# Kernel tuning notes

Hardware: AMD Instinct MI355X
Metric: run time of the kernel (lower is better)

## Reference

```python
import jax, jax.numpy as jnp
import numpy as np

QMAX = 127.0  # int8 symmetric range


def fake_quant(t):
    """Per-tensor symmetric int8 quantize->dequantize (HMQ-style numerics)."""
    scale = jnp.maximum(jnp.max(jnp.abs(t)), 1e-8) / QMAX
    q = jnp.clip(jnp.round(t / scale), -QMAX, QMAX)
    return q * scale


def hmq_linear(x, w, b):
    # quantize activations and weights, dequantized GEMM + bias
    xq = fake_quant(x)
    wq = fake_quant(w)
    return jnp.einsum('bsi,oi->bso', xq, wq) + b


def setup_inputs() -> dict:
    key = jax.random.key(0)
    k = jax.random.split(key, 5)
    d, h = 1024, 4096
    return {
        'x': jax.random.normal(k[0], (4, 4096, d), dtype=jnp.float32),
        'w1': jax.random.normal(k[1], (h, d), dtype=jnp.float32) * 0.02,
        'b1': jax.random.normal(k[2], (h,), dtype=jnp.float32) * 0.02,
        'w2': jax.random.normal(k[3], (d, h), dtype=jnp.float32) * 0.02,
        'b2': jax.random.normal(k[4], (d,), dtype=jnp.float32) * 0.02,
    }


def reference(x, w1, b1, w2, b2):
    h = hmq_linear(x, w1, b1)          # fc1 (quantized)
    h = jax.nn.gelu(h, approximate=False)  # HMQGeLU (exact erf GELU)
    out = hmq_linear(h, w2, b2)        # fc2 (quantized)
    return out
```

## Files before the change

### kernel.cpp

```cpp
#include <hip/hip_runtime.h>
#include <hip/hip_bf16.h>
#include <math.h>
#include <stdint.h>


typedef int    v4i    __attribute__((ext_vector_type(4)));
typedef short  short8 __attribute__((ext_vector_type(8)));
typedef int8_t char8  __attribute__((ext_vector_type(8)));

#define QMAXF 127.0f

__device__ __forceinline__ float gelu_exact(float v) {
    float z = fabsf(v) * 0.70710678118654752440f;
    float t = __builtin_amdgcn_rcpf(fmaf(0.3275911f, z, 1.0f));
    float p = fmaf(fmaf(fmaf(fmaf(1.061405429f, t, -1.453152027f), t,
                             1.421413741f), t, -0.284496736f), t,
                   0.254829592f) * t;
    float e = __expf(-z * z);
    float erfz = fmaf(-p, e, 1.0f);
    float erfv = v < 0.f ? -erfz : erfz;
    return 0.5f * v * (1.0f + erfv);
}

__global__ void init_slots(unsigned int* slots) {
    if (threadIdx.x < 8) slots[threadIdx.x] = 0u;
}

__global__ void absmax_kernel(const float4* __restrict__ t, int n4,
                              unsigned int* __restrict__ slot) {
    float m = 0.f;
    int stride = gridDim.x * blockDim.x;
    for (int i = blockIdx.x * blockDim.x + threadIdx.x; i < n4; i += stride) {
        float4 v = t[i];
        m = fmaxf(m, fmaxf(fmaxf(fabsf(v.x), fabsf(v.y)),
                           fmaxf(fabsf(v.z), fabsf(v.w))));
    }
#pragma unroll
    for (int off = 32; off > 0; off >>= 1)
        m = fmaxf(m, __shfl_xor(m, off));
    if ((threadIdx.x & 63) == 0)
        atomicMax(slot, __float_as_uint(m));
}

__global__ void quant_stage_kernel(const float* __restrict__ x, int kshift,
                                   int nblocks, const float* __restrict__ slot,
                                   int8_t* __restrict__ q) {
    __shared__ float qt[4][1088];
    const float s = fmaxf(*slot, 1e-8f) / QMAXF;
    const int lane = threadIdx.x & 63;
    const int wv   = threadIdx.x >> 6;
    const int wave0 = (blockIdx.x * blockDim.x + threadIdx.x) >> 6;
    const int nwaves = (gridDim.x * blockDim.x) >> 6;
    const int nkb = 1 << kshift;
    const int K = 64 << kshift;
    float* tw = &qt[wv][0];
    for (int wb = wave0; wb < nblocks; wb += nwaves) {
        const int rb = wb >> kshift;
        const int kc = wb & (nkb - 1);
#pragma unroll
        for (int j = 0; j < 4; j++) {
            const int row = rb * 16 + j * 4 + (lane >> 4);
            float4 v = *(const float4*)(x + (size_t)row * K + kc * 64 + (lane & 15) * 4);
            *(float4*)(tw + (j * 4 + (lane >> 4)) * 68 + (lane & 15) * 4) = v;
        }
        int8_t tmp[16];
#pragma unroll
        for (int t = 0; t < 4; t++) {
            float4 v = *(const float4*)(tw + (lane & 15) * 68 + (lane >> 4) * 16 + t * 4);
            tmp[t*4+0] = (int8_t)fminf(fmaxf(rintf(v.x / s), -127.f), 127.f);
            tmp[t*4+1] = (int8_t)fminf(fmaxf(rintf(v.y / s), -127.f), 127.f);
            tmp[t*4+2] = (int8_t)fminf(fmaxf(rintf(v.z / s), -127.f), 127.f);
            tmp[t*4+3] = (int8_t)fminf(fmaxf(rintf(v.w / s), -127.f), 127.f);
        }
        *(int4*)(q + (size_t)wb * 1024 + lane * 16) = *(const int4*)tmp;
    }
}

__global__ void quant_h_kernel(const short8* __restrict__ h16s,
                               const float* __restrict__ tilescale,
                               const float* __restrict__ hslot,
                               char8* __restrict__ q, int n8) {
    const float sh = fmaxf(*hslot, 1e-8f) / QMAXF;
    const float inv = 1.0f / (32767.f * sh);
    int stride = gridDim.x * blockDim.x;
    for (int i = blockIdx.x * blockDim.x + threadIdx.x; i < n8; i += stride) {
        const int blk = i >> 7;
        const int rb = blk >> 6, kc = blk & 63;
        const int tile = (rb >> 3) * 32 + (kc >> 1);
        const float f = tilescale[tile] * inv;
        short8 v = h16s[i];
        char8 o;
#pragma unroll
        for (int j = 0; j < 8; j++)
            o[j] = (int8_t)fminf(fmaxf(rintf((float)v[j] * f), -127.f), 127.f);
        q[i] = o;
    }
}

#define EPI_G1_STORE_I16 0
#define EPI_G1_MAXONLY   1
#define EPI_G1_QUANT     2
#define EPI_G2_OUT       3

template <int N0>
__device__ __forceinline__ void mfma_pair(v4i (&acc)[4][8], v4i (&af)[4],
                                          v4i b0, v4i b1) {
#pragma unroll
    for (int mi = 0; mi < 4; mi++) {
        acc[mi][N0]     = __builtin_amdgcn_mfma_i32_16x16x64_i8(
            af[mi], b0, acc[mi][N0], 0, 0, 0);
        acc[mi][N0 + 1] = __builtin_amdgcn_mfma_i32_16x16x64_i8(
            af[mi], b1, acc[mi][N0 + 1], 0, 0, 0);
    }
}

template <int EPI>
__global__ __launch_bounds__(512, 2) void gemm_i8_kernel(
    const int8_t* __restrict__ A, const int8_t* __restrict__ B,
    int N, int K,
    const float* __restrict__ slotA, const float* __restrict__ slotB,
    const float* __restrict__ bias,
    int16_t* __restrict__ h16_out,
    float* __restrict__ tilescale,
    unsigned int* __restrict__ maxslot,
    const float* __restrict__ hslot,
    int8_t* __restrict__ q_out,
    float* __restrict__ out)
{
    __shared__ __align__(16) int8_t lds[65536];
    __shared__ float red[8];

    const int tid  = threadIdx.x;
    const int lane = tid & 63;
    const int wv   = tid >> 6;
    const int wm   = wv & 3;
    const int wn   = wv >> 2;

    const int bm = blockIdx.x * 256;
    const int bn = blockIdx.y * 256;
    const int nkb = K >> 6;

    const float sAB = (fmaxf(*slotA, 1e-8f) / QMAXF) *
                      (fmaxf(*slotB, 1e-8f) / QMAXF);

    v4i acc[4][8] = {};

    const size_t rbstride = (size_t)nkb * 1024;

    const int8_t* src[4];
#pragma unroll
    for (int j = 0; j < 4; j++) {
        const int c = wv * 4 + j;
        src[j] = (c < 16 ? A + (size_t)((bm >> 4) + c) * rbstride
                         : B + (size_t)((bn >> 4) + (c - 16)) * rbstride)
                 + lane * 16;
    }

    auto STAGE = [&](int buf, int kt) {
#pragma unroll
        for (int j = 0; j < 4; j++) {
            __builtin_amdgcn_global_load_lds(
                (const __attribute__((address_space(1))) unsigned int*)
                    (src[j] + (size_t)kt * 1024),
                (__attribute__((address_space(3))) unsigned int*)
                    (lds + buf * 32768 + (wv * 4 + j) * 1024),
                16, 0, 0);
        }
    };

    STAGE(0, 0);
    STAGE(1, 1);

    for (int kt = 0; kt < nkb; ++kt) {
        const int buf = kt & 1;
        if (kt + 1 < nkb) {
            asm volatile("s_waitcnt vmcnt(4)" ::: "memory");
        } else {
            asm volatile("s_waitcnt vmcnt(0)" ::: "memory");
        }
        __builtin_amdgcn_sched_barrier(0);
        __builtin_amdgcn_s_barrier();
        __builtin_amdgcn_sched_barrier(0);

        const int8_t* pa = lds + buf * 32768 + (wm * 4) * 1024 + lane * 16;
        const int8_t* pb = lds + buf * 32768 + 16384 + (wn * 8) * 1024 + lane * 16;
        v4i af[4], bf[8];
        af[0] = *(const v4i*)(pa + 0 * 1024);
        af[1] = *(const v4i*)(pa + 1 * 1024);
        af[2] = *(const v4i*)(pa + 2 * 1024);
        af[3] = *(const v4i*)(pa + 3 * 1024);
        bf[0] = *(const v4i*)(pb + 0 * 1024);
        bf[1] = *(const v4i*)(pb + 1 * 1024);
        __builtin_amdgcn_sched_barrier(0);
        bf[2] = *(const v4i*)(pb + 2 * 1024);
        bf[3] = *(const v4i*)(pb + 3 * 1024);
        __builtin_amdgcn_sched_barrier(0);
        bf[4] = *(const v4i*)(pb + 4 * 1024);
        bf[5] = *(const v4i*)(pb + 5 * 1024);
        __builtin_amdgcn_sched_barrier(0);
        bf[6] = *(const v4i*)(pb + 6 * 1024);
        bf[7] = *(const v4i*)(pb + 7 * 1024);
        __builtin_amdgcn_sched_barrier(0);

        asm volatile("s_waitcnt lgkmcnt(6)" ::: "memory");
        __builtin_amdgcn_sched_barrier(0);
        __builtin_amdgcn_s_setprio(1);
        mfma_pair<0>(acc, af, bf[0], bf[1]);
        __builtin_amdgcn_s_setprio(0);

        asm volatile("s_waitcnt lgkmcnt(4)" ::: "memory");
        __builtin_amdgcn_sched_barrier(0);
        __builtin_amdgcn_s_setprio(1);
        mfma_pair<2>(acc, af, bf[2], bf[3]);
        __builtin_amdgcn_s_setprio(0);

        asm volatile("s_waitcnt lgkmcnt(2)" ::: "memory");
        __builtin_amdgcn_sched_barrier(0);
        __builtin_amdgcn_s_setprio(1);
        mfma_pair<4>(acc, af, bf[4], bf[5]);
        __builtin_amdgcn_s_setprio(0);

        asm volatile("s_waitcnt lgkmcnt(0)" ::: "memory");
        __builtin_amdgcn_sched_barrier(0);
        if (kt + 2 < nkb) {
            __builtin_amdgcn_s_barrier();
            __builtin_amdgcn_sched_barrier(0);
            STAGE(buf, kt + 2);
        }
        __builtin_amdgcn_s_setprio(1);
        mfma_pair<6>(acc, af, bf[6], bf[7]);
        __builtin_amdgcn_s_setprio(0);
    }

    __syncthreads();

    float sc_q = 0.f;
    if constexpr (EPI == EPI_G1_QUANT) sc_q = fmaxf(*hslot, 1e-8f) / QMAXF;
    float lmax = 0.f;

#pragma unroll
    for (int mi = 0; mi < 4; mi++) {
#pragma unroll
        for (int ni = 0; ni < 8; ni++) {
            const int col = bn + wn * 128 + ni * 16 + (lane & 15);
            const float bv = bias[col];
#pragma unroll
            for (int r = 0; r < 4; r++) {
                float val = (float)acc[mi][ni][r] * sAB + bv;
                if constexpr (EPI == EPI_G2_OUT) {
                    acc[mi][ni][r] = __float_as_int(val);
                } else {
                    float g = gelu_exact(val);
                    lmax = fmaxf(lmax, fabsf(g));
                    acc[mi][ni][r] = __float_as_int(g);
                }
            }
        }
    }

    float enc = 0.f;
    if constexpr (EPI == EPI_G1_STORE_I16 || EPI == EPI_G1_MAXONLY) {
#pragma unroll
        for (int off = 32; off > 0; off >>= 1)
            lmax = fmaxf(lmax, __shfl_xor(lmax, off));
        if (lane == 0) red[wv] = lmax;
        __syncthreads();
        float m = red[0];
#pragma unroll
        for (int i = 1; i < 8; i++) m = fmaxf(m, red[i]);
        if (tid == 0) {
            if constexpr (EPI == EPI_G1_STORE_I16) {
                const int TS = N >> 7;
                const int tr = bm >> 7, tc = bn >> 7;
                tilescale[(size_t)tr * TS + tc]           = m;
                tilescale[(size_t)tr * TS + tc + 1]       = m;
                tilescale[(size_t)(tr + 1) * TS + tc]     = m;
                tilescale[(size_t)(tr + 1) * TS + tc + 1] = m;
            }
            atomicMax(maxslot, __float_as_uint(m));
        }
        enc = 32767.f / fmaxf(m, 1e-20f);
    }

    if constexpr (EPI == EPI_G1_STORE_I16) {
        const int r16 = (lane >> 4) * 4;
        const int c15 = lane & 15;
        int16_t* tl = (int16_t*)lds;
#pragma unroll
        for (int half = 0; half < 2; half++) {
#pragma unroll
            for (int mi = 0; mi < 4; mi++)
#pragma unroll
                for (int nih = 0; nih < 4; nih++) {
                    const int ni = half * 4 + nih;
#pragma unroll
                    for (int r = 0; r < 4; r++) {
                        float g = __int_as_float(acc[mi][ni][r]);
                        tl[wv * 4096 + mi * 1024 + nih * 256 + (r16 + r) * 16 + c15] =
                            (int16_t)rintf(g * enc);
                    }
                }
            const int kc = (bn >> 6) + wn * 2 + half;
#pragma unroll
            for (int mi = 0; mi < 4; mi++) {
                const int rb = (bm >> 4) + wm * 4 + mi;
                int16_t* dst = h16_out + ((size_t)rb * (N >> 6) + kc) * 1024;
                const int16_t* src2 = tl + wv * 4096 + mi * 1024;
                *(int4*)(dst + lane * 8)       = *(const int4*)(src2 + lane * 8);
                *(int4*)(dst + 512 + lane * 8) = *(const int4*)(src2 + 512 + lane * 8);
            }
        }
    } else if constexpr (EPI != EPI_G1_MAXONLY) {
#pragma unroll
        for (int mi = 0; mi < 4; mi++) {
            const int row0 = bm + wm * 64 + mi * 16 + (lane >> 4) * 4;
#pragma unroll
            for (int ni = 0; ni < 8; ni++) {
                const int col = bn + wn * 128 + ni * 16 + (lane & 15);
#pragma unroll
                for (int r = 0; r < 4; r++) {
                    const int row = row0 + r;
                    float g = __int_as_float(acc[mi][ni][r]);
                    if constexpr (EPI == EPI_G2_OUT) {
                        out[(size_t)row * N + col] = g;
                    } else {
                        float qv = fminf(fmaxf(rintf(g / sc_q), -127.f), 127.f);
                        size_t off = ((size_t)(row >> 4) * (N >> 6) + (col >> 6)) * 1024
                                   + ((col >> 4) & 3) * 256 + (row & 15) * 16 + (col & 15);
                        q_out[off] = (int8_t)qv;
                    }
                }
            }
        }
    }
}


extern "C" void kernel_launch(void* const* d_in, const int* in_sizes, int n_in,
                              void* d_out, int out_size, void* d_ws, size_t ws_size,
                              hipStream_t stream) {
    const float* x  = (const float*)d_in[0];
    const float* w1 = (const float*)d_in[1];
    const float* b1 = (const float*)d_in[2];
    const float* w2 = (const float*)d_in[3];
    const float* b2 = (const float*)d_in[4];
    float* out = (float*)d_out;

    const int D = 1024, H = 4096;
    const int Mrows = 4 * 4096;

    uintptr_t ws = (uintptr_t)d_ws;
    unsigned int* slots = (unsigned int*)ws;
    const float* slotf = (const float*)ws;
    float* tiles = (float*)(ws + 256);
    int8_t* xq  = (int8_t*)(ws + 256 + 65536);
    int8_t* w1q = xq + (size_t)Mrows * D;
    int8_t* w2q = w1q + (size_t)H * D;
    int8_t* hq  = w2q + (size_t)D * H;
    int16_t* h16 = (int16_t*)(hq + (size_t)Mrows * H);
    const size_t need_i16 =
        256 + 65536 + (size_t)Mrows * D + 2u * (size_t)H * D +
        (size_t)Mrows * H + (size_t)Mrows * H * sizeof(int16_t);
    const bool use_store = ws_size >= need_i16;

    init_slots<<<dim3(1), dim3(64), 0, stream>>>(slots);
    absmax_kernel<<<dim3(1024), dim3(256), 0, stream>>>(
        (const float4*)x, Mrows * D / 4, slots + 0);
    absmax_kernel<<<dim3(256), dim3(256), 0, stream>>>(
        (const float4*)w1, H * D / 4, slots + 1);
    absmax_kernel<<<dim3(256), dim3(256), 0, stream>>>(
        (const float4*)w2, D * H / 4, slots + 2);

    quant_stage_kernel<<<dim3(1024), dim3(256), 0, stream>>>(
        x, 4, (Mrows / 16) * (D / 64), slotf + 0, xq);
    quant_stage_kernel<<<dim3(256), dim3(256), 0, stream>>>(
        w1, 4, (H / 16) * (D / 64), slotf + 1, w1q);
    quant_stage_kernel<<<dim3(256), dim3(256), 0, stream>>>(
        w2, 6, (D / 16) * (H / 64), slotf + 2, w2q);

    dim3 g1(Mrows / 256, H / 256);
    if (use_store) {
        gemm_i8_kernel<EPI_G1_STORE_I16><<<g1, dim3(512), 0, stream>>>(
            xq, w1q, H, D, slotf + 0, slotf + 1, b1,
            h16, tiles, slots + 3, nullptr, nullptr, nullptr);
        quant_h_kernel<<<dim3(2048), dim3(256), 0, stream>>>(
            (const short8*)h16, tiles, slotf + 3, (char8*)hq, Mrows * H / 8);
    } else {
        gemm_i8_kernel<EPI_G1_MAXONLY><<<g1, dim3(512), 0, stream>>>(
            xq, w1q, H, D, slotf + 0, slotf + 1, b1,
            nullptr, nullptr, slots + 3, nullptr, nullptr, nullptr);
        gemm_i8_kernel<EPI_G1_QUANT><<<g1, dim3(512), 0, stream>>>(
            xq, w1q, H, D, slotf + 0, slotf + 1, b1,
            nullptr, nullptr, nullptr, slotf + 3, hq, nullptr);
    }

    dim3 g2(Mrows / 256, D / 256);
    gemm_i8_kernel<EPI_G2_OUT><<<g2, dim3(512), 0, stream>>>(
        hq, w2q, D, H, slotf + 3, slotf + 2, b2,
        nullptr, nullptr, nullptr, nullptr, nullptr, out);
}
```

Baseline: 469.7 us.

## Split A/B LDS staging and interleave prefetch with per-slice barriers

```diff
diff --git a/kernel.cpp b/kernel.cpp
--- a/kernel.cpp
+++ b/kernel.cpp
@@ -147,33 +147,48 @@
 
     const size_t rbstride = (size_t)nkb * 1024;
 
-    const int8_t* src[4];
-#pragma unroll
-    for (int j = 0; j < 4; j++) {
-        const int c = wv * 4 + j;
-        src[j] = (c < 16 ? A + (size_t)((bm >> 4) + c) * rbstride
-                         : B + (size_t)((bn >> 4) + (c - 16)) * rbstride)
-                 + lane * 16;
-    }
-
-    auto STAGE = [&](int buf, int kt) {
-#pragma unroll
-        for (int j = 0; j < 4; j++) {
+    const int8_t* srcA[2];
+    const int8_t* srcB[2];
+#pragma unroll
+    for (int j = 0; j < 2; j++) {
+        srcA[j] = A + (size_t)((bm >> 4) + wv * 2 + j) * rbstride + lane * 16;
+        srcB[j] = B + (size_t)((bn >> 4) + wv * 2 + j) * rbstride + lane * 16;
+    }
+
+    auto STAGE_A = [&](int buf_, int kt_) {
+#pragma unroll
+        for (int j = 0; j < 2; j++)
             __builtin_amdgcn_global_load_lds(
                 (const __attribute__((address_space(1))) unsigned int*)
-                    (src[j] + (size_t)kt * 1024),
+                    (srcA[j] + (size_t)kt_ * 1024),
                 (__attribute__((address_space(3))) unsigned int*)
-                    (lds + buf * 32768 + (wv * 4 + j) * 1024),
+                    (lds + buf_ * 32768 + (wv * 2 + j) * 1024),
                 16, 0, 0);
-        }
     };
-
-    STAGE(0, 0);
-    STAGE(1, 1);
+    auto STAGE_B = [&](int buf_, int kt_) {
+#pragma unroll
+        for (int j = 0; j < 2; j++)
+            __builtin_amdgcn_global_load_lds(
+                (const __attribute__((address_space(1))) unsigned int*)
+                    (srcB[j] + (size_t)kt_ * 1024),
+                (__attribute__((address_space(3))) unsigned int*)
+                    (lds + buf_ * 32768 + 16384 + (wv * 2 + j) * 1024),
+                16, 0, 0);
+    };
+
+    STAGE_A(0, 0);
+    STAGE_B(0, 0);
+    STAGE_A(1, 1);
 
     for (int kt = 0; kt < nkb; ++kt) {
         const int buf = kt & 1;
+        const int8_t* pa = lds + buf * 32768 + (wm * 4) * 1024 + lane * 16;
+        const int8_t* pb = lds + buf * 32768 + 16384 + (wn * 8) * 1024 + lane * 16;
+        v4i af[4], bf[8];
+
         if (kt + 1 < nkb) {
+            STAGE_B(buf ^ 1, kt + 1);
+            __builtin_amdgcn_sched_barrier(0);
             asm volatile("s_waitcnt vmcnt(4)" ::: "memory");
         } else {
             asm volatile("s_waitcnt vmcnt(0)" ::: "memory");
@@ -181,10 +196,6 @@
         __builtin_amdgcn_sched_barrier(0);
         __builtin_amdgcn_s_barrier();
         __builtin_amdgcn_sched_barrier(0);
-
-        const int8_t* pa = lds + buf * 32768 + (wm * 4) * 1024 + lane * 16;
-        const int8_t* pb = lds + buf * 32768 + 16384 + (wn * 8) * 1024 + lane * 16;
-        v4i af[4], bf[8];
         af[0] = *(const v4i*)(pa + 0 * 1024);
         af[1] = *(const v4i*)(pa + 1 * 1024);
         af[2] = *(const v4i*)(pa + 2 * 1024);
@@ -192,44 +203,51 @@
         bf[0] = *(const v4i*)(pb + 0 * 1024);
         bf[1] = *(const v4i*)(pb + 1 * 1024);
         __builtin_amdgcn_sched_barrier(0);
-        bf[2] = *(const v4i*)(pb + 2 * 1024);
-        bf[3] = *(const v4i*)(pb + 3 * 1024);
-        __builtin_amdgcn_sched_barrier(0);
-        bf[4] = *(const v4i*)(pb + 4 * 1024);
-        bf[5] = *(const v4i*)(pb + 5 * 1024);
-        __builtin_amdgcn_sched_barrier(0);
-        bf[6] = *(const v4i*)(pb + 6 * 1024);
-        bf[7] = *(const v4i*)(pb + 7 * 1024);
-        __builtin_amdgcn_sched_barrier(0);
-
-        asm volatile("s_waitcnt lgkmcnt(6)" ::: "memory");
+        asm volatile("s_waitcnt lgkmcnt(0)" ::: "memory");
         __builtin_amdgcn_sched_barrier(0);
         __builtin_amdgcn_s_setprio(1);
         mfma_pair<0>(acc, af, bf[0], bf[1]);
         __builtin_amdgcn_s_setprio(0);
-
-        asm volatile("s_waitcnt lgkmcnt(4)" ::: "memory");
+        __builtin_amdgcn_sched_barrier(0);
+        __builtin_amdgcn_s_barrier();
+
+        bf[2] = *(const v4i*)(pb + 2 * 1024);
+        bf[3] = *(const v4i*)(pb + 3 * 1024);
+        __builtin_amdgcn_sched_barrier(0);
+        if (kt + 2 < nkb) STAGE_A(buf, kt + 2);
+        __builtin_amdgcn_sched_barrier(0);
+        __builtin_amdgcn_s_barrier();
+        asm volatile("s_waitcnt lgkmcnt(0)" ::: "memory");
         __builtin_amdgcn_sched_barrier(0);
         __builtin_amdgcn_s_setprio(1);
         mfma_pair<2>(acc, af, bf[2], bf[3]);
         __builtin_amdgcn_s_setprio(0);
-
-        asm volatile("s_waitcnt lgkmcnt(2)" ::: "memory");
+        __builtin_amdgcn_sched_barrier(0);
+        __builtin_amdgcn_s_barrier();
+
+        bf[4] = *(const v4i*)(pb + 4 * 1024);
+        bf[5] = *(const v4i*)(pb + 5 * 1024);
+        __builtin_amdgcn_sched_barrier(0);
+        __builtin_amdgcn_s_barrier();
+        asm volatile("s_waitcnt lgkmcnt(0)" ::: "memory");
         __builtin_amdgcn_sched_barrier(0);
         __builtin_amdgcn_s_setprio(1);
         mfma_pair<4>(acc, af, bf[4], bf[5]);
         __builtin_amdgcn_s_setprio(0);
-
+        __builtin_amdgcn_sched_barrier(0);
+        __builtin_amdgcn_s_barrier();
+
+        bf[6] = *(const v4i*)(pb + 6 * 1024);
+        bf[7] = *(const v4i*)(pb + 7 * 1024);
+        __builtin_amdgcn_sched_barrier(0);
+        __builtin_amdgcn_s_barrier();
         asm volatile("s_waitcnt lgkmcnt(0)" ::: "memory");
         __builtin_amdgcn_sched_barrier(0);
-        if (kt + 2 < nkb) {
-            __builtin_amdgcn_s_barrier();
-            __builtin_amdgcn_sched_barrier(0);
-            STAGE(buf, kt + 2);
-        }
         __builtin_amdgcn_s_setprio(1);
         mfma_pair<6>(acc, af, bf[6], bf[7]);
         __builtin_amdgcn_s_setprio(0);
+        __builtin_amdgcn_sched_barrier(0);
+        __builtin_amdgcn_s_barrier();
     }
 
     __syncthreads();
```

Result: slower. 485.1 us (+3.3%).
